# Kernel optimization log

Hardware: AMD Instinct MI355X
Metric: run time of the kernel (lower is better)

## Reference

```python
import jax, jax.numpy as jnp
import numpy as np

KH, KW = 5, 5  # hardcoded in the module's build()


def setup_inputs() -> dict:
    key = jax.random.key(0)
    k1, k2 = jax.random.split(key)
    # inputs are cast to int32 inside call(); use integer-valued floats so the
    # cast is meaningful (pixel-like values in [0, 256)).
    inputs = jax.random.randint(k1, (4, 224, 224, 16), 0, 256).astype(jnp.float32)
    # learned kernel, shape (5, 5, C_in, filters); small signed integer values
    kernel = jax.random.randint(k2, (5, 5, 16, 32), -8, 8).astype(jnp.float32)
    return {"inputs": inputs, "kernel": kernel}


def reference(inputs, kernel):
    # Faithful int32 math: cast inputs and kernel to int32 as in call().
    x = inputs.astype(jnp.int32)            # [B, H, W, C]
    k = kernel.astype(jnp.int32)            # [KH, KW, C, F]
    B, H, W, C = x.shape
    F = k.shape[-1]
    Ho, Wo = H - KH + 1, W - KW + 1         # VALID 2D cross-correlation
    # Per-(channel, filter) conv with NO reduction over channels: fuse the
    # C_in*F separate MyConv2D launches into one vectorized 25-tap accumulation.
    out = jnp.zeros((B, Ho, Wo, C, F), dtype=jnp.int32)
    for i in range(KH):
        for j in range(KW):
            out = out + x[:, i:i + Ho, j:j + Wo, :, None] * k[i, j, :, :]
    # tf.stack(filters, axis=2) then tf.stack(channels, axis=2) produces
    # output layout [B, Ho, C, F, Wo].
    out = jnp.transpose(out, (0, 1, 3, 4, 2))
    return out.astype(jnp.float32)
```

## Files before the change

kernel.cpp:

```cpp
#include <hip/hip_runtime.h>

#define KH 5
#define KW 5
#define CIN 16
#define NF 32
#define H 224
#define W 224
#define HO 220
#define WO 220

__global__ __launch_bounds__(256) void conv2d_perchan_kernel(
    const float* __restrict__ X,
    const float* __restrict__ Kw,
    float* __restrict__ O)
{
    __shared__ float xs[KH * W];

    const int c  = blockIdx.x;
    const int ho = blockIdx.y;
    const int b  = blockIdx.z;
    const int t  = threadIdx.x;

    const float* xbase = X + ((size_t)(b * H + ho) * W) * CIN + c;
    for (int idx = t; idx < KH * W; idx += 256) {
        xs[idx] = xbase[(size_t)idx * CIN];
    }
    __syncthreads();

    const int wave = t >> 6;
    const int lane = t & 63;
    const int wo0  = lane * 4;
    if (lane >= 55) return;

    float xr[KH][8];
#pragma unroll
    for (int i = 0; i < KH; ++i) {
        const float4 xa = *(const float4*)&xs[i * W + wo0];
        const float4 xb = *(const float4*)&xs[i * W + wo0 + 4];
        xr[i][0] = xa.x; xr[i][1] = xa.y; xr[i][2] = xa.z; xr[i][3] = xa.w;
        xr[i][4] = xb.x; xr[i][5] = xb.y; xr[i][6] = xb.z; xr[i][7] = xb.w;
    }

    const float* kwc = Kw + c * NF;
    const size_t orow = (((size_t)(b * HO + ho) * CIN + c) * NF) * WO + wo0;

#pragma unroll 2
    for (int fi = 0; fi < 8; ++fi) {
        const int f = __builtin_amdgcn_readfirstlane(wave * 8 + fi);
        float wk[KH * KW];
#pragma unroll
        for (int tap = 0; tap < KH * KW; ++tap)
            wk[tap] = kwc[(size_t)tap * (CIN * NF) + f];

        float acc0 = 0.f, acc1 = 0.f, acc2 = 0.f, acc3 = 0.f;
#pragma unroll
        for (int i = 0; i < KH; ++i)
#pragma unroll
            for (int j = 0; j < KW; ++j) {
                const float w = wk[i * KW + j];
                acc0 += xr[i][j + 0] * w;
                acc1 += xr[i][j + 1] * w;
                acc2 += xr[i][j + 2] * w;
                acc3 += xr[i][j + 3] * w;
            }

        *(float4*)&O[orow + (size_t)f * WO] = make_float4(acc0, acc1, acc2, acc3);
    }
}

extern "C" void kernel_launch(void* const* d_in, const int* in_sizes, int n_in,
                              void* d_out, int out_size, void* d_ws, size_t ws_size,
                              hipStream_t stream) {
    const float* X  = (const float*)d_in[0];
    const float* Kw = (const float*)d_in[1];
    float* O        = (float*)d_out;

    dim3 grid(CIN, HO, 4);
    conv2d_perchan_kernel<<<grid, 256, 0, stream>>>(X, Kw, O);
}
```

Baseline: 454.0 us.

## Compute four output rows per block and pre-transpose weights for contiguous loads

Each block now computes four output rows, loading eight input rows into shared memory so overlapping rows are reused across outputs rather than reloaded per row. A small pre-kernel transposes the weights into a per-(channel, filter) padded layout, so each filter's 25 taps are read contiguously instead of strided. This raises register pressure (more accumulators and input registers) and adds a second kernel launch. The output write volume is unchanged, so the kernel likely stays write-bound.

Measured after the change: 444.1 us. -2.2%, faster.

```diff
diff --git a/kernel.cpp b/kernel.cpp
--- a/kernel.cpp
+++ b/kernel.cpp
@@ -8,23 +8,37 @@
 #define W 224
 #define HO 220
 #define WO 220
+#define RPB 4
+#define XROWS (RPB + KH - 1)
+#define WPAD 32
 
-__global__ __launch_bounds__(256) void conv2d_perchan_kernel(
+__global__ void transpose_weights(const float* __restrict__ Kw,
+                                  float* __restrict__ Wt) {
+    int idx = blockIdx.x * 256 + threadIdx.x;
+    if (idx < KH * KW * CIN * NF) {
+        const int tap = idx / (CIN * NF);
+        const int rem = idx - tap * (CIN * NF);
+        const int c   = rem >> 5;
+        const int f   = rem & 31;
+        Wt[((size_t)(c * NF) + f) * WPAD + tap] = Kw[idx];
+    }
+}
+
+__global__ __launch_bounds__(256) void conv2d_main(
     const float* __restrict__ X,
-    const float* __restrict__ Kw,
+    const float* __restrict__ Wt,
     float* __restrict__ O)
 {
-    __shared__ float xs[KH * W];
+    __shared__ float xs[XROWS * W];
 
-    const int c  = blockIdx.x;
-    const int ho = blockIdx.y;
-    const int b  = blockIdx.z;
-    const int t  = threadIdx.x;
+    const int c   = blockIdx.x;
+    const int ho0 = blockIdx.y * RPB;
+    const int b   = blockIdx.z;
+    const int t   = threadIdx.x;
 
-    const float* xbase = X + ((size_t)(b * H + ho) * W) * CIN + c;
-    for (int idx = t; idx < KH * W; idx += 256) {
+    const float* xbase = X + ((size_t)(b * H + ho0) * W) * CIN + c;
+    for (int idx = t; idx < XROWS * W; idx += 256)
         xs[idx] = xbase[(size_t)idx * CIN];
-    }
     __syncthreads();
 
     const int wave = t >> 6;
@@ -32,39 +46,55 @@
     const int wo0  = lane * 4;
     if (lane >= 55) return;
 
-    float xr[KH][8];
+    float xr[XROWS][8];
 #pragma unroll
-    for (int i = 0; i < KH; ++i) {
-        const float4 xa = *(const float4*)&xs[i * W + wo0];
-        const float4 xb = *(const float4*)&xs[i * W + wo0 + 4];
-        xr[i][0] = xa.x; xr[i][1] = xa.y; xr[i][2] = xa.z; xr[i][3] = xa.w;
-        xr[i][4] = xb.x; xr[i][5] = xb.y; xr[i][6] = xb.z; xr[i][7] = xb.w;
+    for (int r = 0; r < XROWS; ++r) {
+        const float4 xa = *(const float4*)&xs[r * W + wo0];
+        const float4 xb = *(const float4*)&xs[r * W + wo0 + 4];
+        xr[r][0] = xa.x; xr[r][1] = xa.y; xr[r][2] = xa.z; xr[r][3] = xa.w;
+        xr[r][4] = xb.x; xr[r][5] = xb.y; xr[r][6] = xb.z; xr[r][7] = xb.w;
     }
 
-    const float* kwc = Kw + c * NF;
-    const size_t orow = (((size_t)(b * HO + ho) * CIN + c) * NF) * WO + wo0;
+    size_t obase[RPB];
+#pragma unroll
+    for (int r = 0; r < RPB; ++r)
+        obase[r] = (((size_t)(b * HO + ho0 + r) * CIN + c) * NF) * WO + wo0;
 
-#pragma unroll 2
+    const float* wc = Wt + (size_t)(c * NF) * WPAD;
+
+#pragma unroll 1
     for (int fi = 0; fi < 8; ++fi) {
         const int f = __builtin_amdgcn_readfirstlane(wave * 8 + fi);
+        const float* wp = wc + (size_t)f * WPAD;
         float wk[KH * KW];
 #pragma unroll
         for (int tap = 0; tap < KH * KW; ++tap)
-            wk[tap] = kwc[(size_t)tap * (CIN * NF) + f];
+            wk[tap] = wp[tap];
 
-        float acc0 = 0.f, acc1 = 0.f, acc2 = 0.f, acc3 = 0.f;
+        float acc[RPB][4];
+#pragma unroll
+        for (int r = 0; r < RPB; ++r)
+#pragma unroll
+            for (int q = 0; q < 4; ++q) acc[r][q] = 0.0f;
+
 #pragma unroll
         for (int i = 0; i < KH; ++i)
 #pragma unroll
             for (int j = 0; j < KW; ++j) {
                 const float w = wk[i * KW + j];
-                acc0 += xr[i][j + 0] * w;
-                acc1 += xr[i][j + 1] * w;
-                acc2 += xr[i][j + 2] * w;
-                acc3 += xr[i][j + 3] * w;
+#pragma unroll
+                for (int r = 0; r < RPB; ++r) {
+                    acc[r][0] += xr[r + i][j + 0] * w;
+                    acc[r][1] += xr[r + i][j + 1] * w;
+                    acc[r][2] += xr[r + i][j + 2] * w;
+                    acc[r][3] += xr[r + i][j + 3] * w;
+                }
             }
 
-        *(float4*)&O[orow + (size_t)f * WO] = make_float4(acc0, acc1, acc2, acc3);
+#pragma unroll
+        for (int r = 0; r < RPB; ++r)
+            *(float4*)&O[obase[r] + (size_t)f * WO] =
+                make_float4(acc[r][0], acc[r][1], acc[r][2], acc[r][3]);
     }
 }
 
@@ -74,7 +104,9 @@
     const float* X  = (const float*)d_in[0];
     const float* Kw = (const float*)d_in[1];
     float* O        = (float*)d_out;
+    float* Wt       = (float*)d_ws;
 
-    dim3 grid(CIN, HO, 4);
-    conv2d_perchan_kernel<<<grid, 256, 0, stream>>>(X, Kw, O);
+    transpose_weights<<<dim3(50), 256, 0, stream>>>(Kw, Wt);
+    dim3 grid(CIN, HO / RPB, 4);
+    conv2d_main<<<grid, 256, 0, stream>>>(X, Wt, O);
 }
```
